# Kernel tuning notes

Measured on AMD Instinct MI355X. Metric: run time of the kernel, lower is better.

## Reference

```python
import jax, jax.numpy as jnp
import numpy as np

D = 512      # model_dim
H = 8        # num_heads
HD = D // H  # head_dim = 64
S = 196      # tokens per channel (14x14 grid)
CHANNELS = np.array([2, 4, 6, 4], dtype=np.int32)  # multiplex channels per sample


def setup_inputs() -> dict:
    key = jax.random.key(0)
    ks = jax.random.split(key, 8)
    C = int(CHANNELS.sum())  # 16
    n = lambda k, shp, s=1.0: jax.random.normal(k, shp, dtype=jnp.float32) * s
    return {
        "x_query": n(ks[0], (C, S, D)),
        "x_keyval": n(ks[1], (C, S, D)),
        "pos": n(ks[2], (C, S, D)),
        "channels": CHANNELS,
        "Wq": n(ks[3], (D, D), 0.02), "bq": jnp.zeros((D,), jnp.float32),
        "Wk": n(ks[4], (D, D), 0.02), "bk": jnp.zeros((D,), jnp.float32),
        "Wv": n(ks[5], (D, D), 0.02), "bv": jnp.zeros((D,), jnp.float32),
        "Wo": n(ks[6], (D, D), 0.02), "bo": jnp.zeros((D,), jnp.float32),
    }


def reference(x_query, x_keyval, pos, channels, Wq, bq, Wk, bk, Wv, bv, Wo, bo):
    C, S_, D_ = x_query.shape
    ch = np.asarray(channels)
    # segment id per packed token; segment i has length channels[i]*S (== cu_seq_len blocks)
    seg = np.repeat(np.arange(ch.shape[0]), ch * S_)                # [T] static
    block_mask = seg[:, None] == seg[None, :]                        # [T,T] static bool

    xq = x_query.reshape(-1, D_)   # [T,D]
    xk = x_keyval.reshape(-1, D_)
    p = pos.reshape(-1, D_)

    # positional embedding fused into Q/K before projection (query_pos/key_pos)
    q = ((xq + p) @ Wq + bq).reshape(-1, H, HD)
    k = ((xk + p) @ Wk + bk).reshape(-1, H, HD)
    v = (xk @ Wv + bv).reshape(-1, H, HD)

    scale = 1.0 / np.sqrt(HD)
    scores = jnp.einsum('qhd,khd->hqk', q, k) * scale               # [H,T,T]
    scores = jnp.where(block_mask[None], scores, jnp.float32(-1e30))
    attn = jax.nn.softmax(scores, axis=-1)
    out = jnp.einsum('hqk,khd->qhd', attn, v).reshape(-1, D_)       # [T,D]
    out = out @ Wo + bo
    return out.reshape(C, S_, D_)
```

## Files before the change

kernel.cpp:

```cpp
#include <hip/hip_runtime.h>


typedef short short8 __attribute__((ext_vector_type(8)));
typedef float f32x4 __attribute__((ext_vector_type(4)));

__device__ __forceinline__ float b2f(unsigned short u) {
    union { float f; unsigned int i; } x; x.i = ((unsigned int)u) << 16; return x.f;
}
__device__ __forceinline__ unsigned short f2b(float f) {
    union { float f; unsigned int i; } x; x.f = f;
    unsigned int r = x.i + 0x7fffu + ((x.i >> 16) & 1u);
    return (unsigned short)(r >> 16);
}

#define NE 1605632
#define WE 262144
#define GS 72

__launch_bounds__(256)
__global__ void prep(const float* __restrict__ xq, const float* __restrict__ xk,
                     const float* __restrict__ pos,
                     const float* __restrict__ W0, const float* __restrict__ W1,
                     const float* __restrict__ W2, const float* __restrict__ W3,
                     unsigned short* __restrict__ WF,
                     unsigned short* __restrict__ aqb, unsigned short* __restrict__ akb,
                     unsigned short* __restrict__ xkbb) {
    const int tid = threadIdx.x;
    if (blockIdx.z < 4) {
        if (blockIdx.x >= 128) return;
        const float* W = blockIdx.z == 0 ? W0 : blockIdx.z == 1 ? W1 : blockIdx.z == 2 ? W2 : W3;
        unsigned short* T = WF + (size_t)blockIdx.z * WE;
        const int s = blockIdx.x * 4 + (tid >> 6);
        const int f = s >> 4, t = s & 15;
        const int lane = tid & 63, quad = lane >> 4, l16 = lane & 15;
        short8 o;
        #pragma unroll
        for (int j = 0; j < 8; ++j)
            o[j] = (short)f2b(W[(size_t)(t * 32 + quad * 8 + j) * 512 + f * 16 + l16]);
        *(short8*)(T + (size_t)s * 512 + lane * 8) = o;
    } else {
        const size_t e = ((size_t)blockIdx.x * 256 + tid) * 8;
        f32x4 q0 = *(const f32x4*)(xq + e),  q1 = *(const f32x4*)(xq + e + 4);
        f32x4 k0 = *(const f32x4*)(xk + e),  k1 = *(const f32x4*)(xk + e + 4);
        f32x4 p0 = *(const f32x4*)(pos + e), p1 = *(const f32x4*)(pos + e + 4);
        short8 a, b, c;
        #pragma unroll
        for (int j = 0; j < 4; ++j) {
            a[j] = (short)f2b(q0[j] + p0[j]); a[4 + j] = (short)f2b(q1[j] + p1[j]);
            b[j] = (short)f2b(k0[j] + p0[j]); b[4 + j] = (short)f2b(k1[j] + p1[j]);
            c[j] = (short)f2b(k0[j]);         c[4 + j] = (short)f2b(k1[j]);
        }
        *(short8*)(aqb + e)  = a;
        *(short8*)(akb + e)  = b;
        *(short8*)(xkbb + e) = c;
    }
}

template <bool OUT_F32>
__device__ __forceinline__ void gemm_wave(const unsigned short* __restrict__ A,
                                          const unsigned short* __restrict__ WFw,
                                          const float* __restrict__ bias,
                                          void* __restrict__ C,
                                          int m0, int n0) {
    const int lane = threadIdx.x & 63;
    const int quad = lane >> 4, l16 = lane & 15;
    const int f0 = n0 >> 4;
    const unsigned short* Arow = A + (size_t)(m0 + l16) * 512 + quad * 8;
    const unsigned short* Bbase = WFw + (size_t)lane * 8;

    f32x4 acc[4] = {};
    #pragma unroll 4
    for (int t = 0; t < 16; ++t) {
        short8 af = *(const short8*)(Arow + t * 32);
        #pragma unroll
        for (int nt = 0; nt < 4; ++nt) {
            short8 bf = *(const short8*)(Bbase + (size_t)((f0 + nt) * 16 + t) * 512);
            acc[nt] = __builtin_amdgcn_mfma_f32_16x16x32_bf16(af, bf, acc[nt], 0, 0, 0);
        }
    }
    #pragma unroll
    for (int nt = 0; nt < 4; ++nt) {
        const int col = n0 + nt * 16 + l16;
        const float bv = bias[col];
        #pragma unroll
        for (int r = 0; r < 4; ++r) {
            const int row = m0 + quad * 4 + r;
            float cv = acc[nt][r] + bv;
            if constexpr (OUT_F32) ((float*)C)[(size_t)row * 512 + col] = cv;
            else ((unsigned short*)C)[(size_t)row * 512 + col] = f2b(cv);
        }
    }
}

__launch_bounds__(256)
__global__ void qkv_gemm(const unsigned short* __restrict__ aqb,
                         const unsigned short* __restrict__ akb,
                         const unsigned short* __restrict__ xkbb,
                         const unsigned short* __restrict__ WF,
                         const float* __restrict__ bq, const float* __restrict__ bk,
                         const float* __restrict__ bv,
                         unsigned short* __restrict__ qb, unsigned short* __restrict__ kb,
                         unsigned short* __restrict__ vb) {
    const unsigned short* A; const unsigned short* WFw; const float* bias; unsigned short* C;
    switch (blockIdx.z) {
        case 0:  A = aqb;  WFw = WF;          bias = bq; C = qb; break;
        case 1:  A = akb;  WFw = WF + WE;     bias = bk; C = kb; break;
        default: A = xkbb; WFw = WF + 2 * WE; bias = bv; C = vb; break;
    }
    gemm_wave<false>(A, WFw, bias, C, blockIdx.x * 64 + (threadIdx.x >> 6) * 16,
                     blockIdx.y * 64);
}

__launch_bounds__(256)
__global__ void out_gemm(const unsigned short* __restrict__ A,
                         const unsigned short* __restrict__ WFo,
                         const float* __restrict__ bo, float* __restrict__ out) {
    gemm_wave<true>(A, WFo, bo, out, blockIdx.x * 64 + (threadIdx.x >> 6) * 16,
                    blockIdx.y * 64);
}

__launch_bounds__(256)
__global__ void attn_seg(const unsigned short* __restrict__ q,
                         const unsigned short* __restrict__ k,
                         const unsigned short* __restrict__ v,
                         unsigned short* __restrict__ o) {
    __shared__ __align__(16) unsigned short Ks[64 * GS];
    __shared__ __align__(16) unsigned short Vt[64 * GS];
    __shared__ __align__(16) unsigned short Pb[4][16 * GS];
    const int bx = blockIdx.x, h = blockIdx.y;
    int off, L, qt;
    if (bx < 7)       { off = 0;    L = 392;  qt = bx; }
    else if (bx < 20) { off = 392;  L = 784;  qt = bx - 7; }
    else if (bx < 39) { off = 1176; L = 1176; qt = bx - 20; }
    else              { off = 2352; L = 784;  qt = bx - 39; }
    const int tid = threadIdx.x;
    const int wave = tid >> 6, lane = tid & 63;
    const int quad = lane >> 4, l16 = lane & 15;
    const int hb = h * 64;
    const int lastr = off + L - 1;

    int qrow = off + qt * 64 + wave * 16 + l16;
    if (qrow > lastr) qrow = lastr;
    short8 aq0 = *(const short8*)(q + (size_t)qrow * 512 + hb + quad * 8);
    short8 aq1 = *(const short8*)(q + (size_t)qrow * 512 + hb + 32 + quad * 8);

    const int skey = tid & 63, sd = (tid >> 6) * 16;
    const int ntiles = (L + 63) >> 6;

    float lrow[4] = {0.f, 0.f, 0.f, 0.f};
    f32x4 oacc[4] = {};

    short8 kr0, kr1, vr0, vr1;
    {
        int krow = off + skey;
        kr0 = *(const short8*)(k + (size_t)krow * 512 + hb + sd);
        kr1 = *(const short8*)(k + (size_t)krow * 512 + hb + sd + 8);
        vr0 = *(const short8*)(v + (size_t)krow * 512 + hb + sd);
        vr1 = *(const short8*)(v + (size_t)krow * 512 + hb + sd + 8);
    }
    for (int b = 0; b < ntiles; ++b) {
        __syncthreads();
        *(short8*)(Ks + skey * GS + sd)     = kr0;
        *(short8*)(Ks + skey * GS + sd + 8) = kr1;
        #pragma unroll
        for (int j = 0; j < 8; ++j) {
            Vt[(sd + j) * GS + skey]     = (unsigned short)vr0[j];
            Vt[(sd + 8 + j) * GS + skey] = (unsigned short)vr1[j];
        }
        __syncthreads();
        if (b + 1 < ntiles) {
            int kk = (b + 1) * 64 + skey;
            int krow = off + (kk < L ? kk : L - 1);
            kr0 = *(const short8*)(k + (size_t)krow * 512 + hb + sd);
            kr1 = *(const short8*)(k + (size_t)krow * 512 + hb + sd + 8);
            vr0 = *(const short8*)(v + (size_t)krow * 512 + hb + sd);
            vr1 = *(const short8*)(v + (size_t)krow * 512 + hb + sd + 8);
        }
        f32x4 s[4];
        #pragma unroll
        for (int g = 0; g < 4; ++g) {
            short8 kb0 = *(const short8*)(Ks + (g * 16 + l16) * GS + quad * 8);
            short8 kb1 = *(const short8*)(Ks + (g * 16 + l16) * GS + 32 + quad * 8);
            f32x4 z = {0.f, 0.f, 0.f, 0.f};
            z = __builtin_amdgcn_mfma_f32_16x16x32_bf16(aq0, kb0, z, 0, 0, 0);
            s[g] = __builtin_amdgcn_mfma_f32_16x16x32_bf16(aq1, kb1, z, 0, 0, 0);
        }
        float p[4][4];
        #pragma unroll
        for (int g = 0; g < 4; ++g) {
            const bool valid = (b * 64 + g * 16 + l16) < L;
            #pragma unroll
            for (int r = 0; r < 4; ++r) {
                p[g][r] = valid ? __expf(fminf(s[g][r] * 0.125f, 30.f)) : 0.f;
                lrow[r] += p[g][r];
            }
        }
        #pragma unroll
        for (int g = 0; g < 4; ++g)
            #pragma unroll
            for (int r = 0; r < 4; ++r)
                Pb[wave][(quad * 4 + r) * GS + g * 16 + l16] = f2b(p[g][r]);
        short8 pa0 = *(const short8*)(Pb[wave] + l16 * GS + quad * 8);
        short8 pa1 = *(const short8*)(Pb[wave] + l16 * GS + 32 + quad * 8);
        #pragma unroll
        for (int nt = 0; nt < 4; ++nt) {
            short8 vf0 = *(const short8*)(Vt + (nt * 16 + l16) * GS + quad * 8);
            short8 vf1 = *(const short8*)(Vt + (nt * 16 + l16) * GS + 32 + quad * 8);
            oacc[nt] = __builtin_amdgcn_mfma_f32_16x16x32_bf16(pa0, vf0, oacc[nt], 0, 0, 0);
            oacc[nt] = __builtin_amdgcn_mfma_f32_16x16x32_bf16(pa1, vf1, oacc[nt], 0, 0, 0);
        }
    }
    #pragma unroll
    for (int r = 0; r < 4; ++r) {
        #pragma unroll
        for (int msk = 1; msk < 16; msk <<= 1)
            lrow[r] += __shfl_xor(lrow[r], msk);
    }
    float linv[4];
    #pragma unroll
    for (int r = 0; r < 4; ++r) linv[r] = 1.0f / lrow[r];
    #pragma unroll
    for (int nt = 0; nt < 4; ++nt) {
        #pragma unroll
        for (int r = 0; r < 4; ++r) {
            const int qi = qt * 64 + wave * 16 + quad * 4 + r;
            if (qi < L)
                o[(size_t)(off + qi) * 512 + hb + nt * 16 + l16] = f2b(oacc[nt][r] * linv[r]);
        }
    }
}

extern "C" void kernel_launch(void* const* d_in, const int* in_sizes, int n_in,
                              void* d_out, int out_size, void* d_ws, size_t ws_size,
                              hipStream_t stream) {
    const float* xq  = (const float*)d_in[0];
    const float* xk  = (const float*)d_in[1];
    const float* pos = (const float*)d_in[2];
    const float* Wq = (const float*)d_in[4];
    const float* bq = (const float*)d_in[5];
    const float* Wk = (const float*)d_in[6];
    const float* bk = (const float*)d_in[7];
    const float* Wv = (const float*)d_in[8];
    const float* bv = (const float*)d_in[9];
    const float* Wo = (const float*)d_in[10];
    const float* bo = (const float*)d_in[11];
    float* out = (float*)d_out;

    unsigned short* ws = (unsigned short*)d_ws;
    unsigned short* qb   = ws;
    unsigned short* kb   = ws + NE;
    unsigned short* vb   = ws + (size_t)2 * NE;
    unsigned short* aqb  = ws + (size_t)3 * NE;
    unsigned short* akb  = ws + (size_t)4 * NE;
    unsigned short* xkbb = ws + (size_t)5 * NE;
    unsigned short* WF   = ws + (size_t)6 * NE;

    prep<<<dim3(784, 1, 5), 256, 0, stream>>>(xq, xk, pos, Wq, Wk, Wv, Wo,
                                              WF, aqb, akb, xkbb);
    qkv_gemm<<<dim3(49, 8, 3), 256, 0, stream>>>(aqb, akb, xkbb, WF, bq, bk, bv,
                                                 qb, kb, vb);
    attn_seg<<<dim3(52, 8), 256, 0, stream>>>(qb, kb, vb, qb);
    out_gemm<<<dim3(49, 8), 256, 0, stream>>>(qb, WF + (size_t)3 * WE, bo, out);
}
```

Before: 153.0 us.

## Store K/V in MFMA fragment layout and use single-wave attention blocks

The QKV GEMM epilogue now writes K and V directly into per-head, MFMA-fragment-ordered buffers. This lets the attention kernel load B operands straight from global memory instead of staging and transposing them through shared memory with block barriers. Attention is relaunched as 64-thread blocks, each handling 16 query rows, for 1576 blocks ordered largest segment first to improve balance. In exchange, the GEMM epilogue now does scattered 2-byte stores, and keys are reread from global or L2 memory by every query block.

```diff
diff --git a/kernel.cpp b/kernel.cpp
--- a/kernel.cpp
+++ b/kernel.cpp
@@ -15,7 +15,14 @@
 
 #define NE 1605632
 #define WE 262144
-#define GS 72
+#define PS 40
+
+__device__ __constant__ int seg_off[4] = {0, 392, 1176, 2352};
+__device__ __constant__ int seg_L[4]   = {392, 784, 1176, 784};
+__device__ __constant__ int seg_fb[4]  = {0, 25, 74, 148};
+__device__ __constant__ int seg_cb[4]  = {0, 13, 38, 75};
+__device__ __constant__ int seg_nf[4]  = {25, 49, 74, 49};
+__device__ __constant__ int seg_nc[4]  = {13, 25, 37, 25};
 
 __launch_bounds__(256)
 __global__ void prep(const float* __restrict__ xq, const float* __restrict__ xk,
@@ -56,7 +63,7 @@
     }
 }
 
-template <bool OUT_F32>
+template <int MODE>
 __device__ __forceinline__ void gemm_wave(const unsigned short* __restrict__ A,
                                           const unsigned short* __restrict__ WFw,
                                           const float* __restrict__ bias,
@@ -78,16 +85,43 @@
             acc[nt] = __builtin_amdgcn_mfma_f32_16x16x32_bf16(af, bf, acc[nt], 0, 0, 0);
         }
     }
-    #pragma unroll
-    for (int nt = 0; nt < 4; ++nt) {
-        const int col = n0 + nt * 16 + l16;
-        const float bv = bias[col];
+    if constexpr (MODE == 0 || MODE == 3) {
+        #pragma unroll
+        for (int nt = 0; nt < 4; ++nt) {
+            const int col = n0 + nt * 16 + l16;
+            const float bv = bias[col];
+            #pragma unroll
+            for (int r = 0; r < 4; ++r) {
+                const int row = m0 + quad * 4 + r;
+                float cv = acc[nt][r] + bv;
+                if constexpr (MODE == 3) ((float*)C)[(size_t)row * 512 + col] = cv;
+                else ((unsigned short*)C)[(size_t)row * 512 + col] = f2b(cv);
+            }
+        }
+    } else {
+        unsigned short* F = (unsigned short*)C;
         #pragma unroll
         for (int r = 0; r < 4; ++r) {
-            const int row = m0 + quad * 4 + r;
-            float cv = acc[nt][r] + bv;
-            if constexpr (OUT_F32) ((float*)C)[(size_t)row * 512 + col] = cv;
-            else ((unsigned short*)C)[(size_t)row * 512 + col] = f2b(cv);
+            const int token = m0 + quad * 4 + r;
+            const int seg = token < 392 ? 0 : token < 1176 ? 1 : token < 2352 ? 2 : 3;
+            const int key = token - seg_off[seg];
+            #pragma unroll
+            for (int nt = 0; nt < 4; ++nt) {
+                const int col = n0 + nt * 16 + l16;
+                const unsigned short val = f2b(acc[nt][r] + bias[col]);
+                const int h = col >> 6;
+                if constexpr (MODE == 1) {
+                    const int f  = seg_fb[seg] + (key >> 4), lk = key & 15;
+                    const int dd = col & 63, t = dd >> 5, pos = dd & 31;
+                    F[(size_t)((h * 197 + f) * 2 + t) * 512 + ((pos >> 3) * 16 + lk) * 8 +
+                      (pos & 7)] = val;
+                } else {
+                    const int c  = seg_cb[seg] + (key >> 5);
+                    const int kq = (key & 31) >> 3, kj = key & 7;
+                    const int nt4 = (col & 63) >> 4;
+                    F[(size_t)((h * 100 + c) * 4 + nt4) * 512 + (kq * 16 + l16) * 8 + kj] = val;
+                }
+            }
         }
     }
 }
@@ -99,115 +133,84 @@
                          const unsigned short* __restrict__ WF,
                          const float* __restrict__ bq, const float* __restrict__ bk,
                          const float* __restrict__ bv,
-                         unsigned short* __restrict__ qb, unsigned short* __restrict__ kb,
-                         unsigned short* __restrict__ vb) {
-    const unsigned short* A; const unsigned short* WFw; const float* bias; unsigned short* C;
+                         unsigned short* __restrict__ qb, unsigned short* __restrict__ Kf,
+                         unsigned short* __restrict__ Vf) {
+    const int m0 = blockIdx.x * 64 + (threadIdx.x >> 6) * 16, n0 = blockIdx.y * 64;
     switch (blockIdx.z) {
-        case 0:  A = aqb;  WFw = WF;          bias = bq; C = qb; break;
-        case 1:  A = akb;  WFw = WF + WE;     bias = bk; C = kb; break;
-        default: A = xkbb; WFw = WF + 2 * WE; bias = bv; C = vb; break;
-    }
-    gemm_wave<false>(A, WFw, bias, C, blockIdx.x * 64 + (threadIdx.x >> 6) * 16,
-                     blockIdx.y * 64);
+        case 0:  gemm_wave<0>(aqb,  WF,          bq, qb, m0, n0); break;
+        case 1:  gemm_wave<1>(akb,  WF + WE,     bk, Kf, m0, n0); break;
+        default: gemm_wave<2>(xkbb, WF + 2 * WE, bv, Vf, m0, n0); break;
+    }
 }
 
 __launch_bounds__(256)
 __global__ void out_gemm(const unsigned short* __restrict__ A,
                          const unsigned short* __restrict__ WFo,
                          const float* __restrict__ bo, float* __restrict__ out) {
-    gemm_wave<true>(A, WFo, bo, out, blockIdx.x * 64 + (threadIdx.x >> 6) * 16,
-                    blockIdx.y * 64);
-}
-
-__launch_bounds__(256)
-__global__ void attn_seg(const unsigned short* __restrict__ q,
-                         const unsigned short* __restrict__ k,
-                         const unsigned short* __restrict__ v,
-                         unsigned short* __restrict__ o) {
-    __shared__ __align__(16) unsigned short Ks[64 * GS];
-    __shared__ __align__(16) unsigned short Vt[64 * GS];
-    __shared__ __align__(16) unsigned short Pb[4][16 * GS];
+    gemm_wave<3>(A, WFo, bo, out, blockIdx.x * 64 + (threadIdx.x >> 6) * 16,
+                 blockIdx.y * 64);
+}
+
+__launch_bounds__(64)
+__global__ void attn_frag(const unsigned short* __restrict__ q,
+                          const unsigned short* __restrict__ Kf,
+                          const unsigned short* __restrict__ Vf,
+                          unsigned short* __restrict__ o) {
+    __shared__ __align__(16) unsigned short Pb[16 * PS];
     const int bx = blockIdx.x, h = blockIdx.y;
-    int off, L, qt;
-    if (bx < 7)       { off = 0;    L = 392;  qt = bx; }
-    else if (bx < 20) { off = 392;  L = 784;  qt = bx - 7; }
-    else if (bx < 39) { off = 1176; L = 1176; qt = bx - 20; }
-    else              { off = 2352; L = 784;  qt = bx - 39; }
-    const int tid = threadIdx.x;
-    const int wave = tid >> 6, lane = tid & 63;
+    int seg, qt;
+    if (bx < 74)       { seg = 2; qt = bx; }
+    else if (bx < 123) { seg = 1; qt = bx - 74; }
+    else if (bx < 172) { seg = 3; qt = bx - 123; }
+    else               { seg = 0; qt = bx - 172; }
+    const int off = seg_off[seg], L = seg_L[seg];
+    const int fb0 = seg_fb[seg], cb0 = seg_cb[seg];
+    const int nf = seg_nf[seg], nc = seg_nc[seg];
+    const int lane = threadIdx.x;
     const int quad = lane >> 4, l16 = lane & 15;
     const int hb = h * 64;
+
+    int qrow = off + qt * 16 + l16;
     const int lastr = off + L - 1;
-
-    int qrow = off + qt * 64 + wave * 16 + l16;
     if (qrow > lastr) qrow = lastr;
     short8 aq0 = *(const short8*)(q + (size_t)qrow * 512 + hb + quad * 8);
     short8 aq1 = *(const short8*)(q + (size_t)qrow * 512 + hb + 32 + quad * 8);
 
-    const int skey = tid & 63, sd = (tid >> 6) * 16;
-    const int ntiles = (L + 63) >> 6;
+    const unsigned short* Kh = Kf + (size_t)h * 197 * 1024 + lane * 8;
+    const unsigned short* Vh = Vf + (size_t)h * 100 * 2048 + lane * 8;
 
     float lrow[4] = {0.f, 0.f, 0.f, 0.f};
     f32x4 oacc[4] = {};
 
-    short8 kr0, kr1, vr0, vr1;
-    {
-        int krow = off + skey;
-        kr0 = *(const short8*)(k + (size_t)krow * 512 + hb + sd);
-        kr1 = *(const short8*)(k + (size_t)krow * 512 + hb + sd + 8);
-        vr0 = *(const short8*)(v + (size_t)krow * 512 + hb + sd);
-        vr1 = *(const short8*)(v + (size_t)krow * 512 + hb + sd + 8);
-    }
-    for (int b = 0; b < ntiles; ++b) {
-        __syncthreads();
-        *(short8*)(Ks + skey * GS + sd)     = kr0;
-        *(short8*)(Ks + skey * GS + sd + 8) = kr1;
-        #pragma unroll
-        for (int j = 0; j < 8; ++j) {
-            Vt[(sd + j) * GS + skey]     = (unsigned short)vr0[j];
-            Vt[(sd + 8 + j) * GS + skey] = (unsigned short)vr1[j];
-        }
-        __syncthreads();
-        if (b + 1 < ntiles) {
-            int kk = (b + 1) * 64 + skey;
-            int krow = off + (kk < L ? kk : L - 1);
-            kr0 = *(const short8*)(k + (size_t)krow * 512 + hb + sd);
-            kr1 = *(const short8*)(k + (size_t)krow * 512 + hb + sd + 8);
-            vr0 = *(const short8*)(v + (size_t)krow * 512 + hb + sd);
-            vr1 = *(const short8*)(v + (size_t)krow * 512 + hb + sd + 8);
-        }
-        f32x4 s[4];
-        #pragma unroll
-        for (int g = 0; g < 4; ++g) {
-            short8 kb0 = *(const short8*)(Ks + (g * 16 + l16) * GS + quad * 8);
-            short8 kb1 = *(const short8*)(Ks + (g * 16 + l16) * GS + 32 + quad * 8);
+    for (int c = 0; c < nc; ++c) {
+        float p[2][4];
+        #pragma unroll
+        for (int g = 0; g < 2; ++g) {
+            int fg = 2 * c + g; if (fg > nf - 1) fg = nf - 1;
+            const unsigned short* kp = Kh + (size_t)(fb0 + fg) * 1024;
+            short8 kb0 = *(const short8*)kp;
+            short8 kb1 = *(const short8*)(kp + 512);
             f32x4 z = {0.f, 0.f, 0.f, 0.f};
             z = __builtin_amdgcn_mfma_f32_16x16x32_bf16(aq0, kb0, z, 0, 0, 0);
-            s[g] = __builtin_amdgcn_mfma_f32_16x16x32_bf16(aq1, kb1, z, 0, 0, 0);
-        }
-        float p[4][4];
-        #pragma unroll
-        for (int g = 0; g < 4; ++g) {
-            const bool valid = (b * 64 + g * 16 + l16) < L;
+            z = __builtin_amdgcn_mfma_f32_16x16x32_bf16(aq1, kb1, z, 0, 0, 0);
+            const bool valid = (c * 32 + g * 16 + l16) < L;
             #pragma unroll
             for (int r = 0; r < 4; ++r) {
-                p[g][r] = valid ? __expf(fminf(s[g][r] * 0.125f, 30.f)) : 0.f;
+                p[g][r] = valid ? __expf(fminf(z[r] * 0.125f, 30.f)) : 0.f;
                 lrow[r] += p[g][r];
             }
         }
         #pragma unroll
-        for (int g = 0; g < 4; ++g)
+        for (int g = 0; g < 2; ++g)
             #pragma unroll
             for (int r = 0; r < 4; ++r)
-                Pb[wave][(quad * 4 + r) * GS + g * 16 + l16] = f2b(p[g][r]);
-        short8 pa0 = *(const short8*)(Pb[wave] + l16 * GS + quad * 8);
-        short8 pa1 = *(const short8*)(Pb[wave] + l16 * GS + 32 + quad * 8);
+                Pb[(quad * 4 + r) * PS + g * 16 + l16] = f2b(p[g][r]);
+        short8 pa = *(const short8*)(Pb + l16 * PS + quad * 8);
+        const unsigned short* vp = Vh + (size_t)(cb0 + c) * 2048;
         #pragma unroll
         for (int nt = 0; nt < 4; ++nt) {
-            short8 vf0 = *(const short8*)(Vt + (nt * 16 + l16) * GS + quad * 8);
-            short8 vf1 = *(const short8*)(Vt + (nt * 16 + l16) * GS + 32 + quad * 8);
-            oacc[nt] = __builtin_amdgcn_mfma_f32_16x16x32_bf16(pa0, vf0, oacc[nt], 0, 0, 0);
-            oacc[nt] = __builtin_amdgcn_mfma_f32_16x16x32_bf16(pa1, vf1, oacc[nt], 0, 0, 0);
+            short8 vf = *(const short8*)(vp + nt * 512);
+            oacc[nt] = __builtin_amdgcn_mfma_f32_16x16x32_bf16(pa, vf, oacc[nt], 0, 0, 0);
         }
     }
     #pragma unroll
@@ -223,7 +226,7 @@
     for (int nt = 0; nt < 4; ++nt) {
         #pragma unroll
         for (int r = 0; r < 4; ++r) {
-            const int qi = qt * 64 + wave * 16 + quad * 4 + r;
+            const int qi = qt * 16 + quad * 4 + r;
             if (qi < L)
                 o[(size_t)(off + qi) * 512 + hb + nt * 16 + l16] = f2b(oacc[nt][r] * linv[r]);
         }
@@ -247,18 +250,19 @@
     float* out = (float*)d_out;
 
     unsigned short* ws = (unsigned short*)d_ws;
+    const size_t SL = 2097152;
     unsigned short* qb   = ws;
-    unsigned short* kb   = ws + NE;
-    unsigned short* vb   = ws + (size_t)2 * NE;
-    unsigned short* aqb  = ws + (size_t)3 * NE;
-    unsigned short* akb  = ws + (size_t)4 * NE;
-    unsigned short* xkbb = ws + (size_t)5 * NE;
-    unsigned short* WF   = ws + (size_t)6 * NE;
+    unsigned short* aqb  = ws + SL;
+    unsigned short* akb  = ws + 2 * SL;
+    unsigned short* xkbb = ws + 3 * SL;
+    unsigned short* Kf   = ws + 4 * SL;
+    unsigned short* Vf   = ws + 5 * SL;
+    unsigned short* WF   = ws + 6 * SL;
 
     prep<<<dim3(784, 1, 5), 256, 0, stream>>>(xq, xk, pos, Wq, Wk, Wv, Wo,
                                               WF, aqb, akb, xkbb);
     qkv_gemm<<<dim3(49, 8, 3), 256, 0, stream>>>(aqb, akb, xkbb, WF, bq, bk, bv,
-                                                 qb, kb, vb);
-    attn_seg<<<dim3(52, 8), 256, 0, stream>>>(qb, kb, vb, qb);
+                                                 qb, Kf, Vf);
+    attn_frag<<<dim3(197, 8), 64, 0, stream>>>(qb, Kf, Vf, qb);
     out_gemm<<<dim3(49, 8), 256, 0, stream>>>(qb, WF + (size_t)3 * WE, bo, out);
 }
```

Measured after the change: 156.2 us. +2.1%, slower.
